# Kernel tuning notes

Measured on AMD Instinct MI355X. Metric: run time of the kernel, lower is better.

The kernel has to match this reference:

```python
import jax, jax.numpy as jnp
import numpy as np

N_NODES = 100000
N_EDGES = 800000
C = 64        # in_channels == out_channels
H = 4         # num_heads
LN_EPS = 1e-5
SM_EPS = 1e-8


def setup_inputs() -> dict:
    key = jax.random.key(0)
    ks = jax.random.split(key, 8)
    return {
        "x": jax.random.normal(ks[0], (N_NODES, C), dtype=jnp.float32),
        "edge_index": jax.random.randint(ks[1], (2, N_EDGES), 0, N_NODES, dtype=jnp.int64),
        "edge_time": jax.random.uniform(ks[2], (N_EDGES,), dtype=jnp.float32),
        "current_time": 1,
        "W_w": jax.random.normal(ks[3], (C, C), dtype=jnp.float32) * (1.0 / np.sqrt(C)),
        "W_b": jnp.zeros((C,), dtype=jnp.float32),
        "attn_w": jax.random.normal(ks[4], (2 * C, H), dtype=jnp.float32) * (1.0 / np.sqrt(2 * C)),
        "attn_b": jnp.zeros((H,), dtype=jnp.float32),
        "decay_rate": jnp.full((1,), 0.1, dtype=jnp.float32),
        "proj_w": jax.random.normal(ks[5], (C * H, C), dtype=jnp.float32) * (1.0 / np.sqrt(C * H)),
        "proj_b": jnp.zeros((C,), dtype=jnp.float32),
        "ln_g": jnp.ones((C,), dtype=jnp.float32),
        "ln_b": jnp.zeros((C,), dtype=jnp.float32),
    }


def reference(x, edge_index, edge_time, current_time, W_w, W_b, attn_w, attn_b,
              decay_rate, proj_w, proj_b, ln_g, ln_b):
    num_nodes = x.shape[0]
    src, dst = edge_index[0], edge_index[1]

    # relation-specific transform (same Linear applied to src and dst node sets)
    h = x @ W_w + W_b                       # (N, C)
    h_src = h[src]                          # (E, C) gather
    h_dst = h[dst]                          # (E, C) gather

    # attention: Linear(2C -> H) + LeakyReLU(0.2)
    logits = h_src @ attn_w[:C] + h_dst @ attn_w[C:] + attn_b   # (E, H)
    scores = jax.nn.leaky_relu(logits, negative_slope=0.2)

    # temporal decay: exp(-softplus(lambda) * delta_t), multiplied pre-softmax
    delta_t = jnp.float32(current_time) - edge_time             # (E,)
    lam = jax.nn.softplus(decay_rate[0])
    scores = scores * jnp.exp(-lam * delta_t)[:, None]

    # segmented (per-destination) softmax over incoming edges
    smax = jax.ops.segment_max(scores, dst, num_segments=num_nodes)   # (N, H)
    e = jnp.exp(scores - smax[dst])                                   # (E, H)
    ssum = jax.ops.segment_sum(e, dst, num_segments=num_nodes)        # (N, H)
    attn = e / (ssum[dst] + SM_EPS)                                   # (E, H)

    # per-edge messages (E, C, H) -> (E, C*H), scatter-add to destinations
    msg = (h_src[:, :, None] * attn[:, None, :]).reshape(-1, C * H)
    agg = jax.ops.segment_sum(msg, dst, num_segments=num_nodes)       # (N, C*H)

    # single edge type -> mean over 1 message is identity
    out = agg @ proj_w + proj_b                                       # (N, C)
    # dropout p=0 (eval) -> identity; residual + LayerNorm + ReLU
    z = out + x
    mu = jnp.mean(z, axis=-1, keepdims=True)
    var = jnp.mean(jnp.square(z - mu), axis=-1, keepdims=True)
    y = ln_g * (z - mu) * jax.lax.rsqrt(var + LN_EPS) + ln_b
    return jax.nn.relu(y)
```

## Files before the change

### kernel.cpp

```cpp
#include <hip/hip_runtime.h>


typedef __attribute__((ext_vector_type(8))) short bf16x8;
typedef __attribute__((ext_vector_type(4))) float f32x4;

__device__ __forceinline__ unsigned short f2bf(float f) {
  unsigned int u = __float_as_uint(f);
  u += 0x7FFFu + ((u >> 16) & 1u);
  return (unsigned short)(u >> 16);
}
__device__ __forceinline__ float bf2f(unsigned short s) {
  return __uint_as_float(((unsigned int)s) << 16);
}
__device__ __forceinline__ unsigned int pk(float a, float b) {
  return (unsigned int)f2bf(a) | ((unsigned int)f2bf(b) << 16);
}
__device__ __forceinline__ float bflo(int u) {
  return __uint_as_float(((unsigned int)u) << 16);
}
__device__ __forceinline__ float bfhi(int u) {
  return __uint_as_float(((unsigned int)u) & 0xFFFF0000u);
}

#define FMA4(P, S, R) { P.x = fmaf(S, R.x, P.x); P.y = fmaf(S, R.y, P.y); \
                        P.z = fmaf(S, R.z, P.z); P.w = fmaf(S, R.w, P.w); }

__global__ __launch_bounds__(256) void k_init(const float* __restrict__ Pw,
    unsigned short* __restrict__ Bf, int* __restrict__ deg, int N)
{
  int i = blockIdx.x * 256 + threadIdx.x;
  if (i < N) deg[i] = 0;
  if (i < 16384) {
    int j    = i & 7;
    int lane = (i >> 3) & 63;
    int cb   = (i >> 9) & 3;
    int ks   = i >> 11;
    int k    = ks * 32 + (lane >> 4) * 8 + j;
    int colg = cb * 16 + (lane & 15);
    Bf[i] = f2bf(Pw[(size_t)k * 64 + colg]);
  }
}

__global__ __launch_bounds__(256) void k_hd(const float* __restrict__ x,
    const float* __restrict__ Ww, const float* __restrict__ Wb,
    const float* __restrict__ attn_w, const int* __restrict__ ei,
    unsigned short* __restrict__ h16, float4* __restrict__ u,
    float4* __restrict__ v, int* __restrict__ deg, int* __restrict__ rank,
    int N, int E, int NBn)
{
  if ((int)blockIdx.x >= NBn) {
    int e = (blockIdx.x - NBn) * 256 + threadIdx.x;
    if (e < E) rank[e] = atomicAdd(&deg[ei[E + e]], 1);
    return;
  }
  const int n = blockIdx.x * 256 + threadIdx.x;
  const bool valid = (n < N);
  const int nc = valid ? n : (N - 1);

  float o[64];
  #pragma unroll
  for (int c = 0; c < 64; ++c) o[c] = Wb[c];

  const float* xr = x + (size_t)nc * 64;
  for (int ch = 0; ch < 16; ++ch) {
    float4 xv = *(const float4*)(xr + ch * 4);
    float a[4] = {xv.x, xv.y, xv.z, xv.w};
    #pragma unroll
    for (int kk = 0; kk < 4; ++kk) {
      const float* Wr = Ww + (size_t)(ch * 4 + kk) * 64;
      #pragma unroll
      for (int c = 0; c < 64; ++c)
        o[c] = fmaf(a[kk], Wr[c], o[c]);
    }
  }

  float4 uu = make_float4(0.f, 0.f, 0.f, 0.f);
  float4 vv = make_float4(0.f, 0.f, 0.f, 0.f);
  const float4* aw = (const float4*)attn_w;
  #pragma unroll
  for (int c = 0; c < 64; ++c) {
    float4 r1 = aw[c];
    float4 r2 = aw[64 + c];
    FMA4(uu, o[c], r1);
    FMA4(vv, o[c], r2);
  }

  if (valid) {
    unsigned int* hr = (unsigned int*)(h16 + (size_t)n * 64);
    #pragma unroll
    for (int i = 0; i < 8; ++i) {
      uint4 w;
      w.x = pk(o[i*8+0], o[i*8+1]);
      w.y = pk(o[i*8+2], o[i*8+3]);
      w.z = pk(o[i*8+4], o[i*8+5]);
      w.w = pk(o[i*8+6], o[i*8+7]);
      *(uint4*)(hr + i * 4) = w;
    }
    u[n] = uu;
    v[n] = vv;
  }
}

__global__ __launch_bounds__(256) void scan1(const int* __restrict__ deg,
    int* __restrict__ offs, int* __restrict__ bsums, int N)
{
  int i = blockIdx.x * 256 + threadIdx.x;
  int lane = threadIdx.x & 63;
  int w = threadIdx.x >> 6;
  int v = (i < N) ? deg[i] : 0;
  int s = v;
  #pragma unroll
  for (int d = 1; d < 64; d <<= 1) {
    int t = __shfl_up(s, d, 64);
    if (lane >= d) s += t;
  }
  __shared__ int wsum[4];
  if (lane == 63) wsum[w] = s;
  __syncthreads();
  int add = 0;
  if (w > 0) add += wsum[0];
  if (w > 1) add += wsum[1];
  if (w > 2) add += wsum[2];
  if (i < N) offs[i] = s - v + add;
  if (threadIdx.x == 255) bsums[blockIdx.x] = wsum[0] + wsum[1] + wsum[2] + wsum[3];
}

__global__ __launch_bounds__(512) void scan2(int* bsums, int NB)
{
  __shared__ int lds[512];
  int t = threadIdx.x;
  int v = (t < NB) ? bsums[t] : 0;
  lds[t] = v;
  __syncthreads();
  for (int s = 1; s < 512; s <<= 1) {
    int a = (t >= s) ? lds[t - s] : 0;
    __syncthreads();
    lds[t] += a;
    __syncthreads();
  }
  if (t < NB) bsums[t] = lds[t] - v;
}

__global__ __launch_bounds__(256) void k_fill(const int* __restrict__ ei,
    const float* __restrict__ et, const int* __restrict__ ctime,
    const float* __restrict__ drate, const float4* __restrict__ u,
    const float4* __restrict__ v, const float* __restrict__ attn_b,
    const int* __restrict__ offs, const int* __restrict__ bsums,
    const int* __restrict__ rank, int4* __restrict__ csr, int E)
{
  int e = blockIdx.x * 256 + threadIdx.x;
  if (e >= E) return;
  const int s = ei[e];
  const int d = ei[E + e];
  const float4 us = u[s];
  const float4 vd = v[d];
  const float4 ab = *(const float4*)attn_b;
  const float lam = log1pf(__expf(drate[0]));
  const float w = __expf(-lam * ((float)ctime[0] - et[e]));

  float4 o; float t;
  t = us.x + vd.x + ab.x; t = (t > 0.f ? t : 0.2f * t) * w; o.x = __expf(t);
  t = us.y + vd.y + ab.y; t = (t > 0.f ? t : 0.2f * t) * w; o.y = __expf(t);
  t = us.z + vd.z + ab.z; t = (t > 0.f ? t : 0.2f * t) * w; o.z = __expf(t);
  t = us.w + vd.w + ab.w; t = (t > 0.f ? t : 0.2f * t) * w; o.w = __expf(t);

  int4 rec;
  rec.x = s;
  rec.y = (int)pk(o.x, o.y);
  rec.z = (int)pk(o.z, o.w);
  rec.w = 0;
  csr[offs[d] + bsums[d >> 8] + rank[e]] = rec;
}

__global__ __launch_bounds__(256) void k_agg(const unsigned short* __restrict__ h16,
    const int4* __restrict__ csr, const int* __restrict__ offs,
    const int* __restrict__ bsums, unsigned short* __restrict__ agg,
    int N, int E)
{
  const int c = threadIdx.x & 63;
  const int wid = blockIdx.x * 4 + (threadIdx.x >> 6);
  const int wstride = gridDim.x * 4;

  for (int n0 = wid; n0 < N; n0 += wstride) {
    const int n = __builtin_amdgcn_readfirstlane(n0);
    const int p0 = offs[n] + bsums[n >> 8];
    const int p1 = (n + 1 < N) ? (offs[n + 1] + bsums[(n + 1) >> 8]) : E;
    const int nf = (p1 - p0) & ~3;

    float acc0 = 0.f, acc1 = 0.f, acc2 = 0.f, acc3 = 0.f;
    float den0 = 0.f, den1 = 0.f, den2 = 0.f, den3 = 0.f;

    int4 rA0, rA1, rA2, rA3;
    float gA0 = 0.f, gA1 = 0.f, gA2 = 0.f, gA3 = 0.f;
    if (nf) {
      rA0 = csr[p0];     rA1 = csr[p0 + 1];
      rA2 = csr[p0 + 2]; rA3 = csr[p0 + 3];
      gA0 = bf2f(h16[(size_t)rA0.x * 64 + c]);
      gA1 = bf2f(h16[(size_t)rA1.x * 64 + c]);
      gA2 = bf2f(h16[(size_t)rA2.x * 64 + c]);
      gA3 = bf2f(h16[(size_t)rA3.x * 64 + c]);
    }
    for (int p = p0; p < p0 + nf; p += 4) {
      int4 rB0, rB1, rB2, rB3;
      float gB0, gB1, gB2, gB3;
      const bool more = (p + 4 < p0 + nf);
      if (more) {
        rB0 = csr[p + 4]; rB1 = csr[p + 5];
        rB2 = csr[p + 6]; rB3 = csr[p + 7];
        gB0 = bf2f(h16[(size_t)rB0.x * 64 + c]);
        gB1 = bf2f(h16[(size_t)rB1.x * 64 + c]);
        gB2 = bf2f(h16[(size_t)rB2.x * 64 + c]);
        gB3 = bf2f(h16[(size_t)rB3.x * 64 + c]);
      }
      float e00 = bflo(rA0.y), e01 = bfhi(rA0.y), e02 = bflo(rA0.z), e03 = bfhi(rA0.z);
      float e10 = bflo(rA1.y), e11 = bfhi(rA1.y), e12 = bflo(rA1.z), e13 = bfhi(rA1.z);
      float e20 = bflo(rA2.y), e21 = bfhi(rA2.y), e22 = bflo(rA2.z), e23 = bfhi(rA2.z);
      float e30 = bflo(rA3.y), e31 = bfhi(rA3.y), e32 = bflo(rA3.z), e33 = bfhi(rA3.z);
      den0 += (e00 + e10) + (e20 + e30);
      den1 += (e01 + e11) + (e21 + e31);
      den2 += (e02 + e12) + (e22 + e32);
      den3 += (e03 + e13) + (e23 + e33);
      acc0 = fmaf(e00, gA0, fmaf(e10, gA1, fmaf(e20, gA2, fmaf(e30, gA3, acc0))));
      acc1 = fmaf(e01, gA0, fmaf(e11, gA1, fmaf(e21, gA2, fmaf(e31, gA3, acc1))));
      acc2 = fmaf(e02, gA0, fmaf(e12, gA1, fmaf(e22, gA2, fmaf(e32, gA3, acc2))));
      acc3 = fmaf(e03, gA0, fmaf(e13, gA1, fmaf(e23, gA2, fmaf(e33, gA3, acc3))));
      if (more) {
        rA0 = rB0; rA1 = rB1; rA2 = rB2; rA3 = rB3;
        gA0 = gB0; gA1 = gB1; gA2 = gB2; gA3 = gB3;
      }
    }
    for (int p = p0 + nf; p < p1; ++p) {
      int4 r = csr[p];
      float g = bf2f(h16[(size_t)r.x * 64 + c]);
      float e0 = bflo(r.y), e1 = bfhi(r.y), e2 = bflo(r.z), e3 = bfhi(r.z);
      den0 += e0; den1 += e1; den2 += e2; den3 += e3;
      acc0 = fmaf(e0, g, acc0);
      acc1 = fmaf(e1, g, acc1);
      acc2 = fmaf(e2, g, acc2);
      acc3 = fmaf(e3, g, acc3);
    }
    uint2 w;
    w.x = pk(acc0 / (den0 + 1e-8f), acc1 / (den1 + 1e-8f));
    w.y = pk(acc2 / (den2 + 1e-8f), acc3 / (den3 + 1e-8f));
    *(uint2*)(agg + (size_t)n * 256 + c * 4) = w;
  }
}

__global__ __launch_bounds__(256) void k_projm(const unsigned short* __restrict__ agg,
    const unsigned short* __restrict__ Bf, const float* __restrict__ x,
    const float* __restrict__ Pb,
    const float* __restrict__ lg, const float* __restrict__ lb,
    float* __restrict__ out, int N)
{
  const int lane = threadIdx.x & 63;
  const int wv = threadIdx.x >> 6;
  const int nt = blockIdx.x * 4 + wv;
  if (nt * 16 >= N) return;
  const int col  = lane & 15;
  const int quad = lane >> 4;
  const int base = nt * 16;

  int na = base + col; if (na >= N) na = N - 1;
  const unsigned short* aptr = agg + (size_t)na * 256 + quad * 8;

  f32x4 acc0 = {0.f, 0.f, 0.f, 0.f};
  f32x4 acc1 = {0.f, 0.f, 0.f, 0.f};
  f32x4 acc2 = {0.f, 0.f, 0.f, 0.f};
  f32x4 acc3 = {0.f, 0.f, 0.f, 0.f};

  #pragma unroll
  for (int ks = 0; ks < 8; ++ks) {
    bf16x8 av = *(const bf16x8*)(aptr + ks * 32);
    bf16x8 b0 = *(const bf16x8*)(Bf + ((size_t)(ks * 4 + 0) * 64 + lane) * 8);
    bf16x8 b1 = *(const bf16x8*)(Bf + ((size_t)(ks * 4 + 1) * 64 + lane) * 8);
    bf16x8 b2 = *(const bf16x8*)(Bf + ((size_t)(ks * 4 + 2) * 64 + lane) * 8);
    bf16x8 b3 = *(const bf16x8*)(Bf + ((size_t)(ks * 4 + 3) * 64 + lane) * 8);
    acc0 = __builtin_amdgcn_mfma_f32_16x16x32_bf16(av, b0, acc0, 0, 0, 0);
    acc1 = __builtin_amdgcn_mfma_f32_16x16x32_bf16(av, b1, acc1, 0, 0, 0);
    acc2 = __builtin_amdgcn_mfma_f32_16x16x32_bf16(av, b2, acc2, 0, 0, 0);
    acc3 = __builtin_amdgcn_mfma_f32_16x16x32_bf16(av, b3, acc3, 0, 0, 0);
  }

  const float pb0 = Pb[col], pb1 = Pb[16 + col], pb2 = Pb[32 + col], pb3 = Pb[48 + col];
  float v[4][4];
  #pragma unroll
  for (int r = 0; r < 4; ++r) {
    int node = base + quad * 4 + r; if (node >= N) node = N - 1;
    const float* xr = x + (size_t)node * 64;
    v[0][r] = acc0[r] + pb0 + xr[col];
    v[1][r] = acc1[r] + pb1 + xr[16 + col];
    v[2][r] = acc2[r] + pb2 + xr[32 + col];
    v[3][r] = acc3[r] + pb3 + xr[48 + col];
  }

  float mu[4], inv[4];
  #pragma unroll
  for (int r = 0; r < 4; ++r) {
    float s = (v[0][r] + v[1][r]) + (v[2][r] + v[3][r]);
    s += __shfl_xor(s, 1, 64); s += __shfl_xor(s, 2, 64);
    s += __shfl_xor(s, 4, 64); s += __shfl_xor(s, 8, 64);
    mu[r] = s * 0.015625f;
  }
  #pragma unroll
  for (int r = 0; r < 4; ++r) {
    float d0 = v[0][r] - mu[r], d1 = v[1][r] - mu[r];
    float d2 = v[2][r] - mu[r], d3 = v[3][r] - mu[r];
    float s = fmaf(d0, d0, d1 * d1) + fmaf(d2, d2, d3 * d3);
    s += __shfl_xor(s, 1, 64); s += __shfl_xor(s, 2, 64);
    s += __shfl_xor(s, 4, 64); s += __shfl_xor(s, 8, 64);
    inv[r] = rsqrtf(s * 0.015625f + 1e-5f);
  }

  const float lg0 = lg[col], lg1 = lg[16 + col], lg2 = lg[32 + col], lg3 = lg[48 + col];
  const float lb0 = lb[col], lb1 = lb[16 + col], lb2 = lb[32 + col], lb3 = lb[48 + col];
  #pragma unroll
  for (int r = 0; r < 4; ++r) {
    int node = base + quad * 4 + r;
    if (node < N) {
      float* orow = out + (size_t)node * 64;
      orow[col]      = fmaxf(fmaf(lg0 * (v[0][r] - mu[r]), inv[r], lb0), 0.f);
      orow[16 + col] = fmaxf(fmaf(lg1 * (v[1][r] - mu[r]), inv[r], lb1), 0.f);
      orow[32 + col] = fmaxf(fmaf(lg2 * (v[2][r] - mu[r]), inv[r], lb2), 0.f);
      orow[48 + col] = fmaxf(fmaf(lg3 * (v[3][r] - mu[r]), inv[r], lb3), 0.f);
    }
  }
}

extern "C" void kernel_launch(void* const* d_in, const int* in_sizes, int n_in,
                              void* d_out, int out_size, void* d_ws, size_t ws_size,
                              hipStream_t stream)
{
  const float* x  = (const float*)d_in[0];
  const int*   ei = (const int*)d_in[1];
  const float* et = (const float*)d_in[2];
  const int*   ct = (const int*)d_in[3];
  const float* Ww = (const float*)d_in[4];
  const float* Wb = (const float*)d_in[5];
  const float* aw = (const float*)d_in[6];
  const float* ab = (const float*)d_in[7];
  const float* dr = (const float*)d_in[8];
  const float* Pw = (const float*)d_in[9];
  const float* Pb = (const float*)d_in[10];
  const float* lg = (const float*)d_in[11];
  const float* lb = (const float*)d_in[12];
  float* out = (float*)d_out;

  const int N = in_sizes[0] / 64;
  const int E = in_sizes[2];

  char* ws = (char*)d_ws;
  size_t off = 0;
  auto take = [&](size_t bytes) -> char* {
    char* p = ws + off;
    off = (off + bytes + 255) & ~(size_t)255;
    return p;
  };
  unsigned short* h16 = (unsigned short*)take((size_t)N * 64 * 2);
  int*    deg    = (int*)take((size_t)N * 4);
  int*    offs   = (int*)take((size_t)N * 4);
  int*    bsums  = (int*)take(512 * 4);
  int*    rank   = (int*)take((size_t)E * 4);
  int4*   csr    = (int4*)take((size_t)E * 16);
  unsigned short* agg = (unsigned short*)take((size_t)N * 256 * 2);
  float4* u      = (float4*)take((size_t)N * 16);
  float4* v      = (float4*)take((size_t)N * 16);
  unsigned short* Bf = (unsigned short*)take(16384 * 2);

  const int NBn = (N + 255) / 256;
  const int NBe = (E + 255) / 256;

  k_init<<<NBn, 256, 0, stream>>>(Pw, Bf, deg, N);
  k_hd<<<NBn + NBe, 256, 0, stream>>>(x, Ww, Wb, aw, ei, h16, u, v, deg, rank, N, E, NBn);
  scan1<<<NBn, 256, 0, stream>>>(deg, offs, bsums, N);
  scan2<<<1, 512, 0, stream>>>(bsums, NBn);
  k_fill<<<NBe, 256, 0, stream>>>(ei, et, ct, dr, u, v, ab, offs, bsums, rank, csr, E);
  k_agg<<<2048, 256, 0, stream>>>(h16, csr, offs, bsums, agg, N, E);
  const int NT = (N + 15) / 16;
  k_projm<<<(NT + 3) / 4, 256, 0, stream>>>(agg, Bf, x, Pb, lg, lb, out, N);
}
```

Before: 252.9 us.

## Compute node transform and attention projections with split-bf16 MFMA

```diff
diff --git a/kernel.cpp b/kernel.cpp
--- a/kernel.cpp
+++ b/kernel.cpp
@@ -22,12 +22,59 @@
   return __uint_as_float(((unsigned int)u) & 0xFFFF0000u);
 }
 
-#define FMA4(P, S, R) { P.x = fmaf(S, R.x, P.x); P.y = fmaf(S, R.y, P.y); \
-                        P.z = fmaf(S, R.z, P.z); P.w = fmaf(S, R.w, P.w); }
+__device__ __forceinline__ void split8(float4 a, float4 b, bf16x8* hi, bf16x8* lo) {
+  float f[8] = {a.x, a.y, a.z, a.w, b.x, b.y, b.z, b.w};
+  bf16x8 h, l;
+  #pragma unroll
+  for (int j = 0; j < 8; ++j) {
+    unsigned short hs = f2bf(f[j]);
+    h[j] = (short)hs;
+    l[j] = (short)f2bf(f[j] - bf2f(hs));
+  }
+  *hi = h; *lo = l;
+}
 
 __global__ __launch_bounds__(256) void k_init(const float* __restrict__ Pw,
-    unsigned short* __restrict__ Bf, int* __restrict__ deg, int N)
-{
+    const float* __restrict__ Ww, const float* __restrict__ Wb,
+    const float* __restrict__ aw, unsigned short* __restrict__ Bf,
+    unsigned short* __restrict__ Ah, unsigned short* __restrict__ Al,
+    float* __restrict__ bc, int* __restrict__ deg, int N, int NBn)
+{
+  if ((int)blockIdx.x == NBn) {
+    int t = threadIdx.x;
+    for (int i = t; i < 5120; i += 256) {
+      int j = i & 7, lane = (i >> 3) & 63, ks = (i >> 9) & 1, rb = i >> 10;
+      int row = rb * 16 + (lane & 15);
+      int k   = ks * 32 + (lane >> 4) * 8 + j;
+      float w = 0.f;
+      if (row < 64) {
+        w = Ww[(size_t)k * 64 + row];
+      } else if (row < 72) {
+        int jj = row - 64;
+        const float* ac = (jj < 4) ? (aw + jj) : (aw + 256 + (jj - 4));
+        float s = 0.f;
+        for (int c = 0; c < 64; ++c) s = fmaf(Ww[(size_t)k * 64 + c], ac[c * 4], s);
+        w = s;
+      }
+      unsigned short hh = f2bf(w);
+      Ah[i] = hh;
+      Al[i] = f2bf(w - bf2f(hh));
+    }
+    if (t < 80) {
+      float b = 0.f;
+      if (t < 64) {
+        b = Wb[t];
+      } else if (t < 72) {
+        int jj = t - 64;
+        const float* ac = (jj < 4) ? (aw + jj) : (aw + 256 + (jj - 4));
+        float s = 0.f;
+        for (int c = 0; c < 64; ++c) s = fmaf(Wb[c], ac[c * 4], s);
+        b = s;
+      }
+      bc[t] = b;
+    }
+    return;
+  }
   int i = blockIdx.x * 256 + threadIdx.x;
   if (i < N) deg[i] = 0;
   if (i < 16384) {
@@ -41,63 +88,97 @@
   }
 }
 
-__global__ __launch_bounds__(256) void k_hd(const float* __restrict__ x,
-    const float* __restrict__ Ww, const float* __restrict__ Wb,
-    const float* __restrict__ attn_w, const int* __restrict__ ei,
+#define RBSTEP(ACC, RB) { \
+  bf16x8 fh0 = *(const bf16x8*)(Ah + ((RB * 2 + 0) * 64 + lane) * 8); \
+  bf16x8 fl0 = *(const bf16x8*)(Al + ((RB * 2 + 0) * 64 + lane) * 8); \
+  bf16x8 fh1 = *(const bf16x8*)(Ah + ((RB * 2 + 1) * 64 + lane) * 8); \
+  bf16x8 fl1 = *(const bf16x8*)(Al + ((RB * 2 + 1) * 64 + lane) * 8); \
+  ACC = __builtin_amdgcn_mfma_f32_16x16x32_bf16(fh0, bh0, ACC, 0, 0, 0); \
+  ACC = __builtin_amdgcn_mfma_f32_16x16x32_bf16(fl0, bh0, ACC, 0, 0, 0); \
+  ACC = __builtin_amdgcn_mfma_f32_16x16x32_bf16(fh0, bl0, ACC, 0, 0, 0); \
+  ACC = __builtin_amdgcn_mfma_f32_16x16x32_bf16(fh1, bh1, ACC, 0, 0, 0); \
+  ACC = __builtin_amdgcn_mfma_f32_16x16x32_bf16(fl1, bh1, ACC, 0, 0, 0); \
+  ACC = __builtin_amdgcn_mfma_f32_16x16x32_bf16(fh1, bl1, ACC, 0, 0, 0); \
+}
+
+__global__ __launch_bounds__(256, 4) void k_hd(const float* __restrict__ x,
+    const unsigned short* __restrict__ Ah, const unsigned short* __restrict__ Al,
+    const float* __restrict__ bc, const int* __restrict__ ei,
     unsigned short* __restrict__ h16, float4* __restrict__ u,
     float4* __restrict__ v, int* __restrict__ deg, int* __restrict__ rank,
-    int N, int E, int NBn)
-{
-  if ((int)blockIdx.x >= NBn) {
-    int e = (blockIdx.x - NBn) * 256 + threadIdx.x;
-    if (e < E) rank[e] = atomicAdd(&deg[ei[E + e]], 1);
+    int N, int E, int NBe)
+{
+  if ((int)blockIdx.x < NBe) {
+    int e0 = blockIdx.x * 1024 + threadIdx.x * 4;
+    if (e0 + 3 < E) {
+      int4 d4 = *(const int4*)(ei + E + e0);
+      int4 r4;
+      r4.x = atomicAdd(&deg[d4.x], 1);
+      r4.y = atomicAdd(&deg[d4.y], 1);
+      r4.z = atomicAdd(&deg[d4.z], 1);
+      r4.w = atomicAdd(&deg[d4.w], 1);
+      *(int4*)(rank + e0) = r4;
+    } else {
+      for (int e = e0; e < E; ++e) rank[e] = atomicAdd(&deg[ei[E + e]], 1);
+    }
     return;
   }
-  const int n = blockIdx.x * 256 + threadIdx.x;
-  const bool valid = (n < N);
-  const int nc = valid ? n : (N - 1);
-
-  float o[64];
-  #pragma unroll
-  for (int c = 0; c < 64; ++c) o[c] = Wb[c];
-
-  const float* xr = x + (size_t)nc * 64;
-  for (int ch = 0; ch < 16; ++ch) {
-    float4 xv = *(const float4*)(xr + ch * 4);
-    float a[4] = {xv.x, xv.y, xv.z, xv.w};
-    #pragma unroll
-    for (int kk = 0; kk < 4; ++kk) {
-      const float* Wr = Ww + (size_t)(ch * 4 + kk) * 64;
-      #pragma unroll
-      for (int c = 0; c < 64; ++c)
-        o[c] = fmaf(a[kk], Wr[c], o[c]);
-    }
-  }
-
-  float4 uu = make_float4(0.f, 0.f, 0.f, 0.f);
-  float4 vv = make_float4(0.f, 0.f, 0.f, 0.f);
-  const float4* aw = (const float4*)attn_w;
-  #pragma unroll
-  for (int c = 0; c < 64; ++c) {
-    float4 r1 = aw[c];
-    float4 r2 = aw[64 + c];
-    FMA4(uu, o[c], r1);
-    FMA4(vv, o[c], r2);
-  }
-
-  if (valid) {
-    unsigned int* hr = (unsigned int*)(h16 + (size_t)n * 64);
-    #pragma unroll
-    for (int i = 0; i < 8; ++i) {
-      uint4 w;
-      w.x = pk(o[i*8+0], o[i*8+1]);
-      w.y = pk(o[i*8+2], o[i*8+3]);
-      w.z = pk(o[i*8+4], o[i*8+5]);
-      w.w = pk(o[i*8+6], o[i*8+7]);
-      *(uint4*)(hr + i * 4) = w;
-    }
-    u[n] = uu;
-    v[n] = vv;
+  const int lane = threadIdx.x & 63;
+  const int wv   = threadIdx.x >> 6;
+  const int col  = lane & 15;
+  const int quad = lane >> 4;
+
+  const float4 bc0 = *(const float4*)(bc +  0 + quad * 4);
+  const float4 bc1 = *(const float4*)(bc + 16 + quad * 4);
+  const float4 bc2 = *(const float4*)(bc + 32 + quad * 4);
+  const float4 bc3 = *(const float4*)(bc + 48 + quad * 4);
+  const float4 bc4 = *(const float4*)(bc + 64 + quad * 4);
+
+  const int base0 = (blockIdx.x - NBe) * 256 + wv * 64;
+  for (int st = 0; st < 4; ++st) {
+    const int node = base0 + st * 16 + col;
+    const bool val = (node < N);
+    const int nc = val ? node : N - 1;
+    const float* xr = x + (size_t)nc * 64 + quad * 8;
+    float4 x0 = *(const float4*)(xr);
+    float4 x1 = *(const float4*)(xr + 4);
+    float4 x2 = *(const float4*)(xr + 32);
+    float4 x3 = *(const float4*)(xr + 36);
+    bf16x8 bh0, bl0, bh1, bl1;
+    split8(x0, x1, &bh0, &bl0);
+    split8(x2, x3, &bh1, &bl1);
+
+    f32x4 a0 = {0.f, 0.f, 0.f, 0.f};
+    f32x4 a1 = {0.f, 0.f, 0.f, 0.f};
+    f32x4 a2 = {0.f, 0.f, 0.f, 0.f};
+    f32x4 a3 = {0.f, 0.f, 0.f, 0.f};
+    f32x4 a4 = {0.f, 0.f, 0.f, 0.f};
+    RBSTEP(a0, 0);
+    RBSTEP(a1, 1);
+    RBSTEP(a2, 2);
+    RBSTEP(a3, 3);
+    RBSTEP(a4, 4);
+
+    if (val) {
+      unsigned short* hr = h16 + (size_t)node * 64 + quad * 4;
+      uint2 w0, w1, w2, w3;
+      w0.x = pk(a0[0] + bc0.x, a0[1] + bc0.y);
+      w0.y = pk(a0[2] + bc0.z, a0[3] + bc0.w);
+      w1.x = pk(a1[0] + bc1.x, a1[1] + bc1.y);
+      w1.y = pk(a1[2] + bc1.z, a1[3] + bc1.w);
+      w2.x = pk(a2[0] + bc2.x, a2[1] + bc2.y);
+      w2.y = pk(a2[2] + bc2.z, a2[3] + bc2.w);
+      w3.x = pk(a3[0] + bc3.x, a3[1] + bc3.y);
+      w3.y = pk(a3[2] + bc3.z, a3[3] + bc3.w);
+      *(uint2*)(hr)      = w0;
+      *(uint2*)(hr + 16) = w1;
+      *(uint2*)(hr + 32) = w2;
+      *(uint2*)(hr + 48) = w3;
+      if (quad == 0)
+        u[node] = make_float4(a4[0] + bc4.x, a4[1] + bc4.y, a4[2] + bc4.z, a4[3] + bc4.w);
+      else if (quad == 1)
+        v[node] = make_float4(a4[0] + bc4.x, a4[1] + bc4.y, a4[2] + bc4.z, a4[3] + bc4.w);
+    }
   }
 }
 
@@ -365,12 +446,16 @@
   float4* u      = (float4*)take((size_t)N * 16);
   float4* v      = (float4*)take((size_t)N * 16);
   unsigned short* Bf = (unsigned short*)take(16384 * 2);
-
-  const int NBn = (N + 255) / 256;
-  const int NBe = (E + 255) / 256;
-
-  k_init<<<NBn, 256, 0, stream>>>(Pw, Bf, deg, N);
-  k_hd<<<NBn + NBe, 256, 0, stream>>>(x, Ww, Wb, aw, ei, h16, u, v, deg, rank, N, E, NBn);
+  unsigned short* Ah = (unsigned short*)take(5120 * 2);
+  unsigned short* Al = (unsigned short*)take(5120 * 2);
+  float*  bc     = (float*)take(80 * 4);
+
+  const int NBn  = (N + 255) / 256;
+  const int NBe  = (E + 255) / 256;
+  const int NBe4 = (E + 1023) / 1024;
+
+  k_init<<<NBn + 1, 256, 0, stream>>>(Pw, Ww, Wb, aw, Bf, Ah, Al, bc, deg, N, NBn);
+  k_hd<<<NBe4 + NBn, 256, 0, stream>>>(x, Ah, Al, bc, ei, h16, u, v, deg, rank, N, E, NBe4);
   scan1<<<NBn, 256, 0, stream>>>(deg, offs, bsums, N);
   scan2<<<1, 512, 0, stream>>>(bsums, NBn);
   k_fill<<<NBe, 256, 0, stream>>>(ei, et, ct, dr, u, v, ab, offs, bsums, rank, csr, E);
```

Result: slower. 266.2 us (+5.3%).
